# Kernel tuning notes

Hardware: AMD Instinct MI355X
Metric: run time of the kernel (lower is better)

## Reference

```python
import jax, jax.numpy as jnp
import numpy as np

B, S, D, E = 4, 4096, 2048, 8
T = B * S                      # 16384 tokens
C = int(T / E * 1.25)          # capacity = 2560


def setup_inputs() -> dict:
    key = jax.random.key(0)
    k1, k2, k3 = jax.random.split(key, 3)
    rng = np.random.default_rng(0)
    # each token routed to one expert; overflow tokens beyond capacity are dropped
    expert_of = rng.integers(0, E, T)
    scatter_idx = np.full(E * C, T, dtype=np.int32)   # sentinel T -> dummy row
    dropped_mask = np.zeros(T, dtype=bool)
    for e in range(E):
        idx = np.nonzero(expert_of == e)[0]
        kept = idx[:C]
        scatter_idx[e * C: e * C + kept.size] = kept
        dropped_mask[idx[C:]] = True
    return {
        "expert_outputs": jax.random.normal(k1, (E * C, D), dtype=jnp.float32),
        "x": jax.random.normal(k2, (B, S, D), dtype=jnp.float32),
        "route_prob_max": jax.random.uniform(k3, (T,), dtype=jnp.float32),
        "scatter_idx": jnp.asarray(scatter_idx),
        "dropped_mask": jnp.asarray(dropped_mask),
    }


def reference(expert_outputs, x, route_prob_max, scatter_idx, dropped_mask):
    b, s, d = x.shape
    x_flat = x.reshape(-1, d)                         # [T, D]
    t = x_flat.shape[0]
    # scatter expert outputs to token positions; sentinel index t lands in dummy row
    buf = jnp.zeros((t + 1, d), dtype=x.dtype)
    final = buf.at[scatter_idx].set(expert_outputs)[:t]
    # dropped tokens pass through residual; their routing factor is 1.0
    final = jnp.where(dropped_mask[:, None], x_flat, final)
    factor = jnp.where(dropped_mask, jnp.asarray(1.0, x.dtype), route_prob_max)
    final = final * factor[:, None]
    return final.reshape(b, s, d)   # dropout p=0.0 -> identity
```

## Files before the change

kernel.cpp:

```cpp
#include <hip/hip_runtime.h>

__global__ void moe_combine_kernel(const float4* __restrict__ eo,
                                   const float4* __restrict__ x,
                                   const float* __restrict__ rpm,
                                   const int* __restrict__ scatter_idx,
                                   const unsigned char* __restrict__ dropped,
                                   float4* __restrict__ out,
                                   int n, int T, int D4) {
    int row = blockIdx.y;
    int c = blockIdx.x * blockDim.x + threadIdx.x;

    if (row < n) {
        int t = scatter_idx[row];
        if ((unsigned)t >= (unsigned)T) return;
        float f = rpm[t];
        float4 v = eo[(size_t)row * D4 + c];
        v.x *= f; v.y *= f; v.z *= f; v.w *= f;
        out[(size_t)t * D4 + c] = v;
    } else {
        int t = row - n;
        if (!dropped[t]) return;
        out[(size_t)t * D4 + c] = x[(size_t)t * D4 + c];
    }
}

extern "C" void kernel_launch(void* const* d_in, const int* in_sizes, int n_in,
                              void* d_out, int out_size, void* d_ws, size_t ws_size,
                              hipStream_t stream) {
    const float* eo            = (const float*)d_in[0];
    const float* x             = (const float*)d_in[1];
    const float* rpm           = (const float*)d_in[2];
    const int*   scatter_idx   = (const int*)d_in[3];
    const unsigned char* dmask = (const unsigned char*)d_in[4];

    const int T  = in_sizes[2];
    const int D  = in_sizes[1] / T;
    const int n  = in_sizes[3];
    const int D4 = D / 4;

    dim3 grid((D4 + 255) / 256, n + T);
    moe_combine_kernel<<<grid, 256, 0, stream>>>(
        (const float4*)eo, (const float4*)x, rpm, scatter_idx, dmask,
        (float4*)d_out, n, T, D4);
}
```

Measured before the change: 330.6 us.

## Process multiple rows per block and compact dropped tokens per block

Expert rows are now handled four per block, with each thread striding across the full row, which replaces the 2D grid that had one block column per 256 float4 segment of a row. Dropped-token passthrough now runs one block per 256 tokens: it compacts the dropped indices into shared memory with an atomic counter and then copies those rows. This removes the large number of blocks that only read the mask and exit, and cuts per-block launch overhead. The mask blocks carry an uneven, serial per-block workload, which may leave some blocks as stragglers.

```diff
diff --git a/kernel.cpp b/kernel.cpp
--- a/kernel.cpp
+++ b/kernel.cpp
@@ -1,26 +1,54 @@
 #include <hip/hip_runtime.h>
+
+
+#define ROWS_PER_BLOCK 4
 
 __global__ void moe_combine_kernel(const float4* __restrict__ eo,
                                    const float4* __restrict__ x,
                                    const float* __restrict__ rpm,
-                                   const int* __restrict__ scatter_idx,
-                                   const unsigned char* __restrict__ dropped,
+                                   const int* __restrict__ sidx,
+                                   const unsigned char* __restrict__ dmask,
                                    float4* __restrict__ out,
-                                   int n, int T, int D4) {
-    int row = blockIdx.y;
-    int c = blockIdx.x * blockDim.x + threadIdx.x;
-
-    if (row < n) {
-        int t = scatter_idx[row];
-        if ((unsigned)t >= (unsigned)T) return;
-        float f = rpm[t];
-        float4 v = eo[(size_t)row * D4 + c];
-        v.x *= f; v.y *= f; v.z *= f; v.w *= f;
-        out[(size_t)t * D4 + c] = v;
+                                   int nRowBlocks, int n, int T, int D4) {
+    if ((int)blockIdx.x < nRowBlocks) {
+        int j0 = blockIdx.x * ROWS_PER_BLOCK;
+        #pragma unroll
+        for (int r = 0; r < ROWS_PER_BLOCK; ++r) {
+            int j = j0 + r;
+            if (j < n) {
+                int t = sidx[j];
+                if ((unsigned)t < (unsigned)T) {
+                    float f = rpm[t];
+                    const float4* __restrict__ src = eo + (size_t)j * D4;
+                    float4*       __restrict__ dst = out + (size_t)t * D4;
+                    for (int c = threadIdx.x; c < D4; c += blockDim.x) {
+                        float4 v = src[c];
+                        v.x *= f; v.y *= f; v.z *= f; v.w *= f;
+                        dst[c] = v;
+                    }
+                }
+            }
+        }
     } else {
-        int t = row - n;
-        if (!dropped[t]) return;
-        out[(size_t)t * D4 + c] = x[(size_t)t * D4 + c];
+        int base = (blockIdx.x - nRowBlocks) * blockDim.x;
+        __shared__ int list[256];
+        __shared__ int cnt;
+        if (threadIdx.x == 0) cnt = 0;
+        __syncthreads();
+        int t = base + threadIdx.x;
+        if (t < T && dmask[t]) {
+            int i = atomicAdd(&cnt, 1);
+            if (i < 256) list[i] = t;
+        }
+        __syncthreads();
+        int m = cnt < 256 ? cnt : 256;
+        for (int i = 0; i < m; ++i) {
+            int td = list[i];
+            const float4* __restrict__ src = x + (size_t)td * D4;
+            float4*       __restrict__ dst = out + (size_t)td * D4;
+            for (int c = threadIdx.x; c < D4; c += blockDim.x)
+                dst[c] = src[c];
+        }
     }
 }
 
@@ -38,8 +66,10 @@
     const int n  = in_sizes[3];
     const int D4 = D / 4;
 
-    dim3 grid((D4 + 255) / 256, n + T);
-    moe_combine_kernel<<<grid, 256, 0, stream>>>(
+    const int nRowBlocks  = (n + ROWS_PER_BLOCK - 1) / ROWS_PER_BLOCK;
+    const int nMaskBlocks = (T + 255) / 256;
+
+    moe_combine_kernel<<<nRowBlocks + nMaskBlocks, 256, 0, stream>>>(
         (const float4*)eo, (const float4*)x, rpm, scatter_idx, dmask,
-        (float4*)d_out, n, T, D4);
+        (float4*)d_out, nRowBlocks, n, T, D4);
 }
```

Result: no change. 325.7 us (-1.5%).
